# Kernel tuning notes

Measured on AMD Instinct MI355X. Metric: run time of the kernel, lower is better.

## Reference

```python
import jax, jax.numpy as jnp
import numpy as np
from jax import lax

EPS = 1e-5  # torch BatchNorm2d default


def setup_inputs() -> dict:
    key = jax.random.key(0)
    k1, k2, k3 = jax.random.split(key, 3)
    C = 64
    x = jax.random.normal(k1, (32, C, 128, 128), dtype=jnp.float32)
    # per-channel 3x3 depthwise weights (OIHW with I=1, feature_group_count=C)
    w = jax.random.normal(k2, (C, 1, 3, 3), dtype=jnp.float32) * (1.0 / 3.0)
    b = jax.random.normal(k3, (C,), dtype=jnp.float32) * 0.1
    gamma = jnp.ones((C,), dtype=jnp.float32)
    beta = jnp.zeros((C,), dtype=jnp.float32)
    return {"x": x, "w": w, "b": b, "gamma": gamma, "beta": beta}


def reference(x, w, b, gamma, beta):
    C = x.shape[1]
    # depthwise 3x3 conv, stride 1, padding 1 (same math as C separate Conv2d(1,1,3))
    y = lax.conv_general_dilated(
        x, w,
        window_strides=(1, 1),
        padding=((1, 1), (1, 1)),
        feature_group_count=C,
        dimension_numbers=("NCHW", "OIHW", "NCHW"),
    )
    y = y + b[None, :, None, None]
    # BatchNorm2d(1) per channel in training mode: batch stats over (N, H, W),
    # biased variance, eps=1e-5
    mean = jnp.mean(y, axis=(0, 2, 3), keepdims=True)
    var = jnp.var(y, axis=(0, 2, 3), keepdims=True)
    y_hat = (y - mean) * lax.rsqrt(var + EPS)
    out = y_hat * gamma[None, :, None, None] + beta[None, :, None, None]
    return jax.nn.relu(out)
```

## Files before the change

kernel.cpp:

```cpp
#include <hip/hip_runtime.h>

#define HW        128
#define PLANE     16384
#define NCH       64
#define NB        32
#define NQ        4
#define NPART     8192
#define COUNT_INV (1.0f / 524288.0f)
#define EPSV      1e-5f
#define GRID_C    1024

#define YELEMS    (NB * NCH * PLANE)
#define PART_OFF  (YELEMS / 2)
#define WS_NEED   ((size_t)YELEMS * 2 + 16384 * 4)

typedef float    f4v __attribute__((ext_vector_type(4)));
typedef _Float16 h4v __attribute__((ext_vector_type(4)));

__device__ __forceinline__ void load_win(const float* __restrict__ bp, int r0, int w4,
                                         bool hasL, bool hasR, float (&v)[6][6]) {
#pragma unroll
    for (int i = 0; i < 6; ++i) {
        int g = r0 - 1 + i;
        float4 m = make_float4(0.f, 0.f, 0.f, 0.f);
        if ((unsigned)g < (unsigned)HW)
            m = *(const float4*)(bp + g * HW + w4);
        float l = __shfl_up(m.w, 1);
        float r = __shfl_down(m.x, 1);
        v[i][0] = hasL ? l : 0.f;
        v[i][1] = m.x; v[i][2] = m.y; v[i][3] = m.z; v[i][4] = m.w;
        v[i][5] = hasR ? r : 0.f;
    }
}

__device__ __forceinline__ void conv_row(const float (&tp)[6], const float (&md)[6],
                                         const float (&bt)[6], const float* W,
                                         float bias, float (&acc)[4]) {
#pragma unroll
    for (int j = 0; j < 4; ++j) {
        float a = bias;
        a = fmaf(tp[j],     W[0], a);
        a = fmaf(tp[j + 1], W[1], a);
        a = fmaf(tp[j + 2], W[2], a);
        a = fmaf(md[j],     W[3], a);
        a = fmaf(md[j + 1], W[4], a);
        a = fmaf(md[j + 2], W[5], a);
        a = fmaf(bt[j],     W[6], a);
        a = fmaf(bt[j + 1], W[7], a);
        a = fmaf(bt[j + 2], W[8], a);
        acc[j] = a;
    }
}

__global__ __launch_bounds__(256, 4) void fused(const float* __restrict__ x,
                                                const float* __restrict__ wgt,
                                                const float* __restrict__ bias,
                                                const float* __restrict__ gamma,
                                                const float* __restrict__ beta,
                                                float* __restrict__ partials,
                                                unsigned int* __restrict__ cnt,
                                                float* __restrict__ out) {
    __shared__ float red[8];
    __shared__ float ssh[4];
    const int b   = blockIdx.x;
    const int t   = threadIdx.x;
    const int cg_ = t & 31, rg = t >> 5;
    const int w4  = cg_ * 4;
    const bool hasL = (cg_ != 0), hasR = (cg_ != 31);

#pragma unroll
    for (int pp = 0; pp < 2; ++pp) {
        const int plane = b * 2 + pp;
        const int c = plane & 63, n = plane >> 6;
        const float* bp = x + (size_t)plane * PLANE;

        float W[9];
#pragma unroll
        for (int k = 0; k < 9; ++k) W[k] = wgt[c * 9 + k];
        const float bv = bias[c];

        float sum = 0.f, sq = 0.f;
#pragma unroll
        for (int q = 0; q < 4; ++q) {
            const int r0 = q * 32 + rg * 4;
            float v[6][6];
            load_win(bp, r0, w4, hasL, hasR, v);
#pragma unroll
            for (int k = 0; k < 4; ++k) {
                float acc[4];
                conv_row(v[k], v[k + 1], v[k + 2], W, bv, acc);
#pragma unroll
                for (int j = 0; j < 4; ++j) {
                    sum += acc[j];
                    sq = fmaf(acc[j], acc[j], sq);
                }
            }
        }
#pragma unroll
        for (int off = 32; off; off >>= 1) {
            sum += __shfl_down(sum, off);
            sq  += __shfl_down(sq, off);
        }
        if ((t & 63) == 0) { red[t >> 6] = sum; red[4 + (t >> 6)] = sq; }
        __syncthreads();
        if (t == 0) {
            partials[c * 32 + n]        = red[0] + red[1] + red[2] + red[3];
            partials[2048 + c * 32 + n] = red[4] + red[5] + red[6] + red[7];
        }
        __syncthreads();
    }

    if (t == 0) {
        __threadfence();
        __hip_atomic_fetch_add(cnt, 1u, __ATOMIC_ACQ_REL, __HIP_MEMORY_SCOPE_AGENT);
        while (__hip_atomic_load(cnt, __ATOMIC_ACQUIRE, __HIP_MEMORY_SCOPE_AGENT)
               < (unsigned)GRID_C) {
            __builtin_amdgcn_s_sleep(8);
        }
    }
    __syncthreads();

    {
        const int c0 = (b * 2) & 63;
        const int c1 = (b * 2 + 1) & 63;
        if (t < 32) {
            float S = partials[c0 * 32 + t];
            float Q = partials[2048 + c0 * 32 + t];
#pragma unroll
            for (int off = 16; off; off >>= 1) {
                S += __shfl_xor(S, off);
                Q += __shfl_xor(Q, off);
            }
            if (t == 0) {
                float mean = S * COUNT_INV;
                float var  = fmaxf(Q * COUNT_INV - mean * mean, 0.f);
                float s    = gamma[c0] * rsqrtf(var + EPSV);
                ssh[0] = s;
                ssh[1] = beta[c0] - mean * s;
            }
        } else if (t >= 64 && t < 96) {
            const int l = t - 64;
            float S = partials[c1 * 32 + l];
            float Q = partials[2048 + c1 * 32 + l];
#pragma unroll
            for (int off = 16; off; off >>= 1) {
                S += __shfl_xor(S, off);
                Q += __shfl_xor(Q, off);
            }
            if (l == 0) {
                float mean = S * COUNT_INV;
                float var  = fmaxf(Q * COUNT_INV - mean * mean, 0.f);
                float s    = gamma[c1] * rsqrtf(var + EPSV);
                ssh[2] = s;
                ssh[3] = beta[c1] - mean * s;
            }
        }
    }
    __syncthreads();

#pragma unroll
    for (int pp = 0; pp < 2; ++pp) {
        const int plane = b * 2 + pp;
        const int c = plane & 63;
        const float* bp = x + (size_t)plane * PLANE;
        float* op = out + (size_t)plane * PLANE;

        float W[9];
#pragma unroll
        for (int k = 0; k < 9; ++k) W[k] = wgt[c * 9 + k];
        const float s  = ssh[pp * 2];
        const float sh = fmaf(bias[c], s, ssh[pp * 2 + 1]);

#pragma unroll
        for (int q = 0; q < 4; ++q) {
            const int r0 = q * 32 + rg * 4;
            float v[6][6];
            load_win(bp, r0, w4, hasL, hasR, v);
#pragma unroll
            for (int k = 0; k < 4; ++k) {
                float acc[4];
                conv_row(v[k], v[k + 1], v[k + 2], W, 0.f, acc);
                f4v o;
                o.x = fmaxf(fmaf(acc[0], s, sh), 0.f);
                o.y = fmaxf(fmaf(acc[1], s, sh), 0.f);
                o.z = fmaxf(fmaf(acc[2], s, sh), 0.f);
                o.w = fmaxf(fmaf(acc[3], s, sh), 0.f);
                __builtin_nontemporal_store(o, (f4v*)(op + (r0 + k) * HW + w4));
            }
        }
    }
}

__device__ __forceinline__ void load_win_fb(const float* __restrict__ bp, int r0, int w4,
                                            bool hasL, bool hasR, float (&v)[6][6]) {
#pragma unroll
    for (int i = 0; i < 6; ++i) {
        int g = r0 - 1 + i;
        if ((unsigned)g < (unsigned)HW) {
            const float* rp = bp + g * HW + w4;
            float4 m = *(const float4*)rp;
            v[i][0] = hasL ? rp[-1] : 0.f;
            v[i][1] = m.x; v[i][2] = m.y; v[i][3] = m.z; v[i][4] = m.w;
            v[i][5] = hasR ? rp[4] : 0.f;
        } else {
#pragma unroll
            for (int j = 0; j < 6; ++j) v[i][j] = 0.f;
        }
    }
}

__global__ __launch_bounds__(256) void pass_conv_stats(const float* __restrict__ x,
                                                       const float* __restrict__ wgt,
                                                       const float* __restrict__ bias,
                                                       _Float16* __restrict__ yh,
                                                       float* __restrict__ partials) {
    __shared__ float red[8];
    const int bid   = blockIdx.x;
    const int q     = bid & 3;
    const int plane = bid >> 2;
    const int c     = plane & 63;
    const int n     = plane >> 6;
    const int t     = threadIdx.x;
    const int cg    = t & 31, rg = t >> 5;
    const int w4    = cg * 4, r0 = q * 32 + rg * 4;
    const bool hasL = (cg != 0), hasR = (cg != 31);

    float W[9];
#pragma unroll
    for (int k = 0; k < 9; ++k) W[k] = wgt[c * 9 + k];
    const float bv = bias[c];
    const float* bp = x + (size_t)plane * PLANE;
    _Float16* yp = yh + (size_t)plane * PLANE;

    float v[6][6];
    load_win_fb(bp, r0, w4, hasL, hasR, v);

    float sum = 0.f, sq = 0.f;
#pragma unroll
    for (int k = 0; k < 4; ++k) {
        float acc[4];
        conv_row(v[k], v[k + 1], v[k + 2], W, bv, acc);
        h4v hv;
        hv.x = (_Float16)acc[0]; hv.y = (_Float16)acc[1];
        hv.z = (_Float16)acc[2]; hv.w = (_Float16)acc[3];
        *(h4v*)(yp + (r0 + k) * HW + w4) = hv;
#pragma unroll
        for (int j = 0; j < 4; ++j) { sum += acc[j]; sq = fmaf(acc[j], acc[j], sq); }
    }
#pragma unroll
    for (int off = 32; off; off >>= 1) {
        sum += __shfl_down(sum, off);
        sq  += __shfl_down(sq, off);
    }
    const int wave = t >> 6, lane = t & 63;
    if (lane == 0) { red[wave] = sum; red[4 + wave] = sq; }
    __syncthreads();
    if (t == 0) {
        const int pi = n * 4 + q;
        partials[c * 128 + pi]         = red[0] + red[1] + red[2] + red[3];
        partials[NPART + c * 128 + pi] = red[4] + red[5] + red[6] + red[7];
    }
}

__global__ __launch_bounds__(256) void pass_norm(const _Float16* __restrict__ yh,
                                                 const float* __restrict__ partials,
                                                 const float* __restrict__ gamma,
                                                 const float* __restrict__ beta,
                                                 float* __restrict__ out) {
    const int bid   = blockIdx.x;
    const int q     = bid & 3;
    const int plane = bid >> 2;
    const int c     = plane & 63;
    const int t     = threadIdx.x;
    const int cg    = t & 31, rg = t >> 5;
    const int w4    = cg * 4, r0 = q * 32 + rg * 4;

    const _Float16* yp = yh + (size_t)plane * PLANE;
    h4v hv[4];
#pragma unroll
    for (int k = 0; k < 4; ++k)
        hv[k] = *(const h4v*)(yp + (r0 + k) * HW + w4);

    const int lane = t & 63;
    float S = partials[c * 128 + lane]         + partials[c * 128 + 64 + lane];
    float Q = partials[NPART + c * 128 + lane] + partials[NPART + c * 128 + 64 + lane];
#pragma unroll
    for (int off = 32; off; off >>= 1) {
        S += __shfl_xor(S, off);
        Q += __shfl_xor(Q, off);
    }
    const float mean = S * COUNT_INV;
    const float var  = fmaxf(Q * COUNT_INV - mean * mean, 0.f);
    const float s    = gamma[c] * rsqrtf(var + EPSV);
    const float sh   = beta[c] - mean * s;

    float* op = out + (size_t)plane * PLANE;
#pragma unroll
    for (int k = 0; k < 4; ++k) {
        f4v o;
        o.x = fmaxf(fmaf((float)hv[k].x, s, sh), 0.f);
        o.y = fmaxf(fmaf((float)hv[k].y, s, sh), 0.f);
        o.z = fmaxf(fmaf((float)hv[k].z, s, sh), 0.f);
        o.w = fmaxf(fmaf((float)hv[k].w, s, sh), 0.f);
        __builtin_nontemporal_store(o, (f4v*)(op + (r0 + k) * HW + w4));
    }
}

extern "C" void kernel_launch(void* const* d_in, const int* in_sizes, int n_in,
                              void* d_out, int out_size, void* d_ws, size_t ws_size,
                              hipStream_t stream) {
    const float* x     = (const float*)d_in[0];
    const float* w     = (const float*)d_in[1];
    const float* b     = (const float*)d_in[2];
    const float* gamma = (const float*)d_in[3];
    const float* beta  = (const float*)d_in[4];
    float* out = (float*)d_out;

    int nb = 0;
    hipError_t qe = hipOccupancyMaxActiveBlocksPerMultiprocessor(
        &nb, reinterpret_cast<const void*>(fused), 256, 0);

    bool coop_ok = false;
    if (qe == hipSuccess && nb >= 4) {
        float* parts      = (float*)d_ws;
        unsigned int* cnt = (unsigned int*)((float*)d_ws + 4096);
        hipMemsetAsync(cnt, 0, sizeof(unsigned int), stream);
        const float* xa = x; const float* wa = w; const float* ba = b;
        const float* ga = gamma; const float* be = beta;
        float* pw = parts; unsigned int* ca = cnt; float* oa = out;
        void* args[] = {&xa, &wa, &ba, &ga, &be, &pw, &ca, &oa};
        hipError_t le = hipLaunchCooperativeKernel(
            reinterpret_cast<const void*>(fused), dim3(GRID_C), dim3(256),
            args, 0, stream);
        coop_ok = (le == hipSuccess);
    }

    if (!coop_ok && ws_size >= WS_NEED) {
        _Float16* yh  = (_Float16*)d_ws;
        float* parts  = (float*)d_ws + PART_OFF;
        pass_conv_stats<<<NB * NCH * NQ, 256, 0, stream>>>(x, w, b, yh, parts);
        pass_norm<<<NB * NCH * NQ, 256, 0, stream>>>(yh, parts, gamma, beta, out);
    }
}
```

Baseline: 73.01 us.

## Cache conv outputs as fp16 in LDS and registers instead of recomputing

The persistent fused kernel now keeps the fp16 conv results of one plane in shared memory (32 KB) and of a second plane in registers across the grid barrier. After the barrier it only applies scale, shift and ReLU to these cached values, instead of re-reading x and redoing the 3x3 conv. The block-to-plane mapping changes so each block handles two planes of the same channel (b and b+1024), which needs only one channel reduction. Halo loads switch from shuffles to direct scalar loads. In exchange, fp16 rounding of intermediates reduces accuracy, and the extra LDS and register pressure may lower occupancy, which the co-resident grid barrier depends on.

```diff
diff --git a/kernel.cpp b/kernel.cpp
--- a/kernel.cpp
+++ b/kernel.cpp
@@ -15,21 +15,25 @@
 #define WS_NEED   ((size_t)YELEMS * 2 + 16384 * 4)
 
 typedef float    f4v __attribute__((ext_vector_type(4)));
+typedef _Float16 h2v __attribute__((ext_vector_type(2)));
 typedef _Float16 h4v __attribute__((ext_vector_type(4)));
+typedef _Float16 h8v __attribute__((ext_vector_type(8)));
 
 __device__ __forceinline__ void load_win(const float* __restrict__ bp, int r0, int w4,
                                          bool hasL, bool hasR, float (&v)[6][6]) {
 #pragma unroll
     for (int i = 0; i < 6; ++i) {
         int g = r0 - 1 + i;
-        float4 m = make_float4(0.f, 0.f, 0.f, 0.f);
-        if ((unsigned)g < (unsigned)HW)
-            m = *(const float4*)(bp + g * HW + w4);
-        float l = __shfl_up(m.w, 1);
-        float r = __shfl_down(m.x, 1);
-        v[i][0] = hasL ? l : 0.f;
-        v[i][1] = m.x; v[i][2] = m.y; v[i][3] = m.z; v[i][4] = m.w;
-        v[i][5] = hasR ? r : 0.f;
+        if ((unsigned)g < (unsigned)HW) {
+            const float* rp = bp + g * HW + w4;
+            float4 m = *(const float4*)rp;
+            v[i][0] = hasL ? rp[-1] : 0.f;
+            v[i][1] = m.x; v[i][2] = m.y; v[i][3] = m.z; v[i][4] = m.w;
+            v[i][5] = hasR ? rp[4] : 0.f;
+        } else {
+#pragma unroll
+            for (int j = 0; j < 6; ++j) v[i][j] = 0.f;
+        }
     }
 }
 
@@ -52,6 +56,61 @@
     }
 }
 
+#define SUMACC(acc)                                                            \
+    { sum += acc[0] + acc[1] + acc[2] + acc[3];                                \
+      sq = fmaf(acc[0], acc[0], sq); sq = fmaf(acc[1], acc[1], sq);            \
+      sq = fmaf(acc[2], acc[2], sq); sq = fmaf(acc[3], acc[3], sq); }
+
+#define PH1B(Q, YA, YB_)                                                       \
+    {                                                                          \
+        const int r0 = (Q) * 32 + rg * 4;                                      \
+        float v[6][6];                                                         \
+        load_win(bpB, r0, w4, hasL, hasR, v);                                  \
+        float acc[4];                                                          \
+        conv_row(v[0], v[1], v[2], W, bv, acc);                                \
+        YA[0] = (_Float16)acc[0]; YA[1] = (_Float16)acc[1];                    \
+        YA[2] = (_Float16)acc[2]; YA[3] = (_Float16)acc[3];                    \
+        SUMACC(acc)                                                            \
+        conv_row(v[1], v[2], v[3], W, bv, acc);                                \
+        YA[4] = (_Float16)acc[0]; YA[5] = (_Float16)acc[1];                    \
+        YA[6] = (_Float16)acc[2]; YA[7] = (_Float16)acc[3];                    \
+        SUMACC(acc)                                                            \
+        conv_row(v[2], v[3], v[4], W, bv, acc);                                \
+        YB_[0] = (_Float16)acc[0]; YB_[1] = (_Float16)acc[1];                  \
+        YB_[2] = (_Float16)acc[2]; YB_[3] = (_Float16)acc[3];                  \
+        SUMACC(acc)                                                            \
+        conv_row(v[3], v[4], v[5], W, bv, acc);                                \
+        YB_[4] = (_Float16)acc[0]; YB_[5] = (_Float16)acc[1];                  \
+        YB_[6] = (_Float16)acc[2]; YB_[7] = (_Float16)acc[3];                  \
+        SUMACC(acc)                                                            \
+    }
+
+#define PH2B(Q, YA, YB_)                                                       \
+    {                                                                          \
+        const int r0 = (Q) * 32 + rg * 4;                                      \
+        f4v o;                                                                 \
+        o.x = fmaxf(fmaf((float)YA[0], s, sh), 0.f);                           \
+        o.y = fmaxf(fmaf((float)YA[1], s, sh), 0.f);                           \
+        o.z = fmaxf(fmaf((float)YA[2], s, sh), 0.f);                           \
+        o.w = fmaxf(fmaf((float)YA[3], s, sh), 0.f);                           \
+        __builtin_nontemporal_store(o, (f4v*)(opB + (r0 + 0) * HW + w4));      \
+        o.x = fmaxf(fmaf((float)YA[4], s, sh), 0.f);                           \
+        o.y = fmaxf(fmaf((float)YA[5], s, sh), 0.f);                           \
+        o.z = fmaxf(fmaf((float)YA[6], s, sh), 0.f);                           \
+        o.w = fmaxf(fmaf((float)YA[7], s, sh), 0.f);                           \
+        __builtin_nontemporal_store(o, (f4v*)(opB + (r0 + 1) * HW + w4));      \
+        o.x = fmaxf(fmaf((float)YB_[0], s, sh), 0.f);                          \
+        o.y = fmaxf(fmaf((float)YB_[1], s, sh), 0.f);                          \
+        o.z = fmaxf(fmaf((float)YB_[2], s, sh), 0.f);                          \
+        o.w = fmaxf(fmaf((float)YB_[3], s, sh), 0.f);                          \
+        __builtin_nontemporal_store(o, (f4v*)(opB + (r0 + 2) * HW + w4));      \
+        o.x = fmaxf(fmaf((float)YB_[4], s, sh), 0.f);                          \
+        o.y = fmaxf(fmaf((float)YB_[5], s, sh), 0.f);                          \
+        o.z = fmaxf(fmaf((float)YB_[6], s, sh), 0.f);                          \
+        o.w = fmaxf(fmaf((float)YB_[7], s, sh), 0.f);                          \
+        __builtin_nontemporal_store(o, (f4v*)(opB + (r0 + 3) * HW + w4));      \
+    }
+
 __global__ __launch_bounds__(256, 4) void fused(const float* __restrict__ x,
                                                 const float* __restrict__ wgt,
                                                 const float* __restrict__ bias,
@@ -60,25 +119,24 @@
                                                 float* __restrict__ partials,
                                                 unsigned int* __restrict__ cnt,
                                                 float* __restrict__ out) {
+    __shared__ unsigned int ylds[32 * 256];
     __shared__ float red[8];
-    __shared__ float ssh[4];
+    __shared__ float ssh[2];
     const int b   = blockIdx.x;
+    const int c   = b & 63;
+    const int nA  = b >> 6;
     const int t   = threadIdx.x;
     const int cg_ = t & 31, rg = t >> 5;
     const int w4  = cg_ * 4;
     const bool hasL = (cg_ != 0), hasR = (cg_ != 31);
 
-#pragma unroll
-    for (int pp = 0; pp < 2; ++pp) {
-        const int plane = b * 2 + pp;
-        const int c = plane & 63, n = plane >> 6;
-        const float* bp = x + (size_t)plane * PLANE;
-
-        float W[9];
-#pragma unroll
-        for (int k = 0; k < 9; ++k) W[k] = wgt[c * 9 + k];
-        const float bv = bias[c];
-
+    float W[9];
+#pragma unroll
+    for (int k = 0; k < 9; ++k) W[k] = wgt[c * 9 + k];
+    const float bv = bias[c];
+
+    {
+        const float* bp = x + (size_t)b * PLANE;
         float sum = 0.f, sq = 0.f;
 #pragma unroll
         for (int q = 0; q < 4; ++q) {
@@ -89,11 +147,12 @@
             for (int k = 0; k < 4; ++k) {
                 float acc[4];
                 conv_row(v[k], v[k + 1], v[k + 2], W, bv, acc);
-#pragma unroll
-                for (int j = 0; j < 4; ++j) {
-                    sum += acc[j];
-                    sq = fmaf(acc[j], acc[j], sq);
-                }
+                h2v p0, p1;
+                p0.x = (_Float16)acc[0]; p0.y = (_Float16)acc[1];
+                p1.x = (_Float16)acc[2]; p1.y = (_Float16)acc[3];
+                ylds[(q * 8 + k * 2) * 256 + t]     = __builtin_bit_cast(unsigned int, p0);
+                ylds[(q * 8 + k * 2 + 1) * 256 + t] = __builtin_bit_cast(unsigned int, p1);
+                SUMACC(acc)
             }
         }
 #pragma unroll
@@ -104,8 +163,30 @@
         if ((t & 63) == 0) { red[t >> 6] = sum; red[4 + (t >> 6)] = sq; }
         __syncthreads();
         if (t == 0) {
-            partials[c * 32 + n]        = red[0] + red[1] + red[2] + red[3];
-            partials[2048 + c * 32 + n] = red[4] + red[5] + red[6] + red[7];
+            partials[c * 32 + nA]        = red[0] + red[1] + red[2] + red[3];
+            partials[2048 + c * 32 + nA] = red[4] + red[5] + red[6] + red[7];
+        }
+        __syncthreads();
+    }
+
+    h8v y0, y1, y2, y3, y4, y5, y6, y7;
+    {
+        const float* bpB = x + (size_t)(b + 1024) * PLANE;
+        float sum = 0.f, sq = 0.f;
+        PH1B(0, y0, y1)
+        PH1B(1, y2, y3)
+        PH1B(2, y4, y5)
+        PH1B(3, y6, y7)
+#pragma unroll
+        for (int off = 32; off; off >>= 1) {
+            sum += __shfl_down(sum, off);
+            sq  += __shfl_down(sq, off);
+        }
+        if ((t & 63) == 0) { red[t >> 6] = sum; red[4 + (t >> 6)] = sq; }
+        __syncthreads();
+        if (t == 0) {
+            partials[c * 32 + nA + 16]        = red[0] + red[1] + red[2] + red[3];
+            partials[2048 + c * 32 + nA + 16] = red[4] + red[5] + red[6] + red[7];
         }
         __syncthreads();
     }
@@ -120,92 +201,51 @@
     }
     __syncthreads();
 
+    if (t < 32) {
+        float S = partials[c * 32 + t];
+        float Q = partials[2048 + c * 32 + t];
+#pragma unroll
+        for (int off = 16; off; off >>= 1) {
+            S += __shfl_xor(S, off);
+            Q += __shfl_xor(Q, off);
+        }
+        if (t == 0) {
+            float mean = S * COUNT_INV;
+            float var  = fmaxf(Q * COUNT_INV - mean * mean, 0.f);
+            float s    = gamma[c] * rsqrtf(var + EPSV);
+            ssh[0] = s;
+            ssh[1] = beta[c] - mean * s;
+        }
+    }
+    __syncthreads();
+    const float s  = ssh[0];
+    const float sh = ssh[1];
+
     {
-        const int c0 = (b * 2) & 63;
-        const int c1 = (b * 2 + 1) & 63;
-        if (t < 32) {
-            float S = partials[c0 * 32 + t];
-            float Q = partials[2048 + c0 * 32 + t];
-#pragma unroll
-            for (int off = 16; off; off >>= 1) {
-                S += __shfl_xor(S, off);
-                Q += __shfl_xor(Q, off);
+        float* op = out + (size_t)b * PLANE;
+#pragma unroll
+        for (int q = 0; q < 4; ++q) {
+#pragma unroll
+            for (int k = 0; k < 4; ++k) {
+                h2v p0 = __builtin_bit_cast(h2v, ylds[(q * 8 + k * 2) * 256 + t]);
+                h2v p1 = __builtin_bit_cast(h2v, ylds[(q * 8 + k * 2 + 1) * 256 + t]);
+                f4v o;
+                o.x = fmaxf(fmaf((float)p0.x, s, sh), 0.f);
+                o.y = fmaxf(fmaf((float)p0.y, s, sh), 0.f);
+                o.z = fmaxf(fmaf((float)p1.x, s, sh), 0.f);
+                o.w = fmaxf(fmaf((float)p1.y, s, sh), 0.f);
+                const int row = q * 32 + rg * 4 + k;
+                __builtin_nontemporal_store(o, (f4v*)(op + row * HW + w4));
             }
-            if (t == 0) {
-                float mean = S * COUNT_INV;
-                float var  = fmaxf(Q * COUNT_INV - mean * mean, 0.f);
-                float s    = gamma[c0] * rsqrtf(var + EPSV);
-                ssh[0] = s;
-                ssh[1] = beta[c0] - mean * s;
-            }
-        } else if (t >= 64 && t < 96) {
-            const int l = t - 64;
-            float S = partials[c1 * 32 + l];
-            float Q = partials[2048 + c1 * 32 + l];
-#pragma unroll
-            for (int off = 16; off; off >>= 1) {
-                S += __shfl_xor(S, off);
-                Q += __shfl_xor(Q, off);
-            }
-            if (l == 0) {
-                float mean = S * COUNT_INV;
-                float var  = fmaxf(Q * COUNT_INV - mean * mean, 0.f);
-                float s    = gamma[c1] * rsqrtf(var + EPSV);
-                ssh[2] = s;
-                ssh[3] = beta[c1] - mean * s;
-            }
-        }
-    }
-    __syncthreads();
-
-#pragma unroll
-    for (int pp = 0; pp < 2; ++pp) {
-        const int plane = b * 2 + pp;
-        const int c = plane & 63;
-        const float* bp = x + (size_t)plane * PLANE;
-        float* op = out + (size_t)plane * PLANE;
-
-        float W[9];
-#pragma unroll
-        for (int k = 0; k < 9; ++k) W[k] = wgt[c * 9 + k];
-        const float s  = ssh[pp * 2];
-        const float sh = fmaf(bias[c], s, ssh[pp * 2 + 1]);
-
-#pragma unroll
-        for (int q = 0; q < 4; ++q) {
-            const int r0 = q * 32 + rg * 4;
-            float v[6][6];
-            load_win(bp, r0, w4, hasL, hasR, v);
-#pragma unroll
-            for (int k = 0; k < 4; ++k) {
-                float acc[4];
-                conv_row(v[k], v[k + 1], v[k + 2], W, 0.f, acc);
-                f4v o;
-                o.x = fmaxf(fmaf(acc[0], s, sh), 0.f);
-                o.y = fmaxf(fmaf(acc[1], s, sh), 0.f);
-                o.z = fmaxf(fmaf(acc[2], s, sh), 0.f);
-                o.w = fmaxf(fmaf(acc[3], s, sh), 0.f);
-                __builtin_nontemporal_store(o, (f4v*)(op + (r0 + k) * HW + w4));
-            }
-        }
-    }
-}
-
-__device__ __forceinline__ void load_win_fb(const float* __restrict__ bp, int r0, int w4,
-                                            bool hasL, bool hasR, float (&v)[6][6]) {
-#pragma unroll
-    for (int i = 0; i < 6; ++i) {
-        int g = r0 - 1 + i;
-        if ((unsigned)g < (unsigned)HW) {
-            const float* rp = bp + g * HW + w4;
-            float4 m = *(const float4*)rp;
-            v[i][0] = hasL ? rp[-1] : 0.f;
-            v[i][1] = m.x; v[i][2] = m.y; v[i][3] = m.z; v[i][4] = m.w;
-            v[i][5] = hasR ? rp[4] : 0.f;
-        } else {
-#pragma unroll
-            for (int j = 0; j < 6; ++j) v[i][j] = 0.f;
-        }
+        }
+    }
+
+    {
+        float* opB = out + (size_t)(b + 1024) * PLANE;
+        PH2B(0, y0, y1)
+        PH2B(1, y2, y3)
+        PH2B(2, y4, y5)
+        PH2B(3, y6, y7)
     }
 }
 
@@ -233,7 +273,7 @@
     _Float16* yp = yh + (size_t)plane * PLANE;
 
     float v[6][6];
-    load_win_fb(bp, r0, w4, hasL, hasR, v);
+    load_win(bp, r0, w4, hasL, hasR, v);
 
     float sum = 0.f, sq = 0.f;
 #pragma unroll
@@ -244,8 +284,7 @@
         hv.x = (_Float16)acc[0]; hv.y = (_Float16)acc[1];
         hv.z = (_Float16)acc[2]; hv.w = (_Float16)acc[3];
         *(h4v*)(yp + (r0 + k) * HW + w4) = hv;
-#pragma unroll
-        for (int j = 0; j < 4; ++j) { sum += acc[j]; sq = fmaf(acc[j], acc[j], sq); }
+        SUMACC(acc)
     }
 #pragma unroll
     for (int off = 32; off; off >>= 1) {
```

New measurement: 72.81 us. No clear change (-0.3%).
